# Kernel tuning notes

Hardware: AMD Instinct MI355X
Metric: run time of the kernel (lower is better)

The kernel has to match this reference:

```python
import jax, jax.numpy as jnp
import numpy as np

WS = (7, 7)          # window size
N = WS[0] * WS[1]    # 49 tokens per window
C = 128              # dim
H = 4                # num heads
D = C // H           # head dim = 32
B = 8192             # batch * num_windows
NW = 1024            # windows per image
SCALE = D ** -0.5


def _relative_position_index():
    coords_h = np.arange(WS[0])
    coords_w = np.arange(WS[1])
    coords = np.stack(np.meshgrid(coords_h, coords_w, indexing='ij'))  # [2,Wh,Ww]
    flat = coords.reshape(2, -1)                                        # [2,N]
    rel = flat[:, :, None] - flat[:, None, :]                           # [2,N,N]
    rel = rel.transpose(1, 2, 0).astype(np.int64)                       # [N,N,2]
    rel[:, :, 0] += WS[0] - 1
    rel[:, :, 1] += WS[1] - 1
    rel[:, :, 0] *= 2 * WS[1] - 1
    return rel.sum(-1)                                                  # [N,N]


def setup_inputs() -> dict:
    key = jax.random.key(0)
    ks = jax.random.split(key, 8)
    s = 0.02
    return {
        'x': jax.random.normal(ks[0], (B, N, C), jnp.float32),
        'y': jax.random.normal(ks[1], (B, N, C), jnp.float32),
        'mask': jnp.zeros((NW, N, N), jnp.float32),
        'Wq': jax.random.normal(ks[2], (C, C), jnp.float32) * s,
        'bq': jnp.zeros((C,), jnp.float32),
        'Wkv': jax.random.normal(ks[3], (C, 2 * C), jnp.float32) * s,
        'bkv': jnp.zeros((2 * C,), jnp.float32),
        'bias_table': jax.random.normal(ks[4], ((2 * WS[0] - 1) * (2 * WS[1] - 1), H), jnp.float32) * s,
        'Wp': jax.random.normal(ks[5], (C, C), jnp.float32) * s,
        'bp': jnp.zeros((C,), jnp.float32),
        'rel_idx': jnp.asarray(_relative_position_index(), jnp.int32),
    }


def reference(x, y, mask, Wq, bq, Wkv, bkv, bias_table, Wp, bp, rel_idx):
    b = x.shape[0]
    # q/kv projections
    q = (x @ Wq + bq).reshape(b, N, H, D).transpose(0, 2, 1, 3) * SCALE   # [B,H,N,D]
    kv = (y @ Wkv + bkv).reshape(b, N, 2, H, D).transpose(2, 0, 3, 1, 4)  # [2,B,H,N,D]
    k, v = kv[0], kv[1]
    attn = jnp.einsum('bhnd,bhmd->bhnm', q, k)                            # [B,H,N,N]
    # relative position bias gather
    bias = bias_table[rel_idx.reshape(-1)].reshape(N, N, H).transpose(2, 0, 1)  # [H,N,N]
    attn = attn + bias[None]
    # mask add per window
    nW = mask.shape[0]
    attn = attn.reshape(b // nW, nW, H, N, N) + mask[None, :, None]
    attn = attn.reshape(b, H, N, N)
    attn = jax.nn.softmax(attn, axis=-1)
    out = jnp.einsum('bhnm,bhmd->bhnd', attn, v)                          # [B,H,N,D]
    out = out.transpose(0, 2, 1, 3).reshape(b, N, C)
    return out @ Wp + bp
```

## Files before the change

kernel.cpp:

```cpp
#include <hip/hip_runtime.h>
#include <cstddef>


#define MFMA16 __builtin_amdgcn_mfma_f32_16x16x32_bf16

typedef float f32x4 __attribute__((ext_vector_type(4)));
typedef __bf16 bf16x8 __attribute__((ext_vector_type(8)));
typedef __bf16 bf16x4 __attribute__((ext_vector_type(4)));

constexpr int NTOK = 49;
constexpr int CDIM = 128;
constexpr int NWIN = 1024;
constexpr int NB = 8192;
constexpr float SCALE_F = 0.17677669529663687f;

__device__ __forceinline__ int sw128(int row, int col) {
  return (row << 8) + ((((col >> 3) ^ row) & 15) << 4) + ((col & 7) << 1);
}
__device__ __forceinline__ int sw64(int row, int col) {
  return (row << 7) + ((((col >> 3) ^ (row >> 1)) & 7) << 4) + ((col & 7) << 1);
}
__device__ __forceinline__ int swp(int m, int nl) {
  return (m << 6) + ((((nl >> 3) ^ (m >> 1)) & 3) << 4) + ((nl & 7) << 1);
}

__global__ void prepack_kernel(const float* __restrict__ Wq, const float* __restrict__ Wkv,
                               const float* __restrict__ Wp, const float* __restrict__ bias_table,
                               const int* __restrict__ rel_idx,
                               unsigned short* __restrict__ wFrag, float* __restrict__ biasM) {
  int t = blockIdx.x * 256 + threadIdx.x;
  if (t < 8192) {
    const int mat = t >> 11;
    const int g = t & 2047;
    const int frag = g >> 6, lane = g & 63;
    const int nt = frag >> 2, ks = frag & 3;
    const int li = lane & 15, q4 = lane >> 4;
    const int n = nt * 16 + li;
    bf16x8 tmp;
#pragma unroll
    for (int j = 0; j < 8; ++j) {
      const int k = ks * 32 + q4 * 8 + j;
      float v;
      if (mat == 0) v = Wq[k * 128 + n];
      else if (mat == 1) v = Wkv[k * 256 + n];
      else if (mat == 2) v = Wkv[k * 256 + 128 + n];
      else v = Wp[k * 128 + n];
      tmp[j] = (__bf16)v;
    }
    *(bf16x8*)(wFrag + (size_t)t * 8) = tmp;
  } else {
    const int tb = t - 8192;
    if (tb < 4 * 49 * 64) {
      const int h = tb / 3136;
      const int rem = tb - h * 3136;
      const int m = rem >> 6, n = rem & 63;
      float v = 0.f;
      if (n < NTOK) v = bias_table[rel_idx[m * 49 + n] * 4 + h];
      biasM[tb] = v;
    }
  }
}

__global__ void bmsum_kernel(const float* __restrict__ mask, const float* __restrict__ bias_table,
                             const int* __restrict__ rel_idx, float* __restrict__ bmSum) {
  __shared__ float smk[2401];
  __shared__ int ri[2401];
  __shared__ float bt[169 * 4];
  const int w = blockIdx.x;
  for (int i = threadIdx.x; i < 2401; i += 256) {
    smk[i] = mask[(size_t)w * 2401 + i];
    ri[i] = rel_idx[i];
  }
  for (int i = threadIdx.x; i < 676; i += 256) bt[i] = bias_table[i];
  __syncthreads();
  for (int i = threadIdx.x; i < 3136; i += 256) {
    const int m = i >> 6, n = i & 63;
    const bool valid = (n < NTOK);
    const int mi = m * 49 + (valid ? n : 0);
    const float base = smk[mi];
    const int r = ri[mi];
#pragma unroll
    for (int h = 0; h < 4; ++h) {
      bmSum[((size_t)w * 4 + h) * 3136 + i] = valid ? (bt[r * 4 + h] + base) : -1e30f;
    }
  }
}

template <bool PRESUM>
__global__ __launch_bounds__(256, 3) void attn_kernel(
    const float* __restrict__ x, const float* __restrict__ y, const float* __restrict__ maskp,
    const float* __restrict__ bq, const float* __restrict__ bkv, const float* __restrict__ bp,
    const unsigned short* __restrict__ wFrag, const float* __restrict__ biasM,
    float* __restrict__ out) {
  __shared__ __align__(16) unsigned char lds[32768];
  const int tid = threadIdx.x;
  const int w = tid >> 6;
  const int lane = tid & 63;
  const int li = lane & 15;
  const int q4 = lane >> 4;
  const int b = blockIdx.x;
  const int mh = w >> 1;
  const int nh = w & 1;

  bf16x8 ax[2][4], ay[2][4];
#pragma unroll
  for (int t = 0; t < 2; ++t) {
    const int mrow = mh * 32 + t * 16 + li;
    const int mm = mrow < NTOK ? mrow : 0;
    const float* xr = x + ((size_t)b * NTOK + mm) * CDIM;
    const float* yr = y + ((size_t)b * NTOK + mm) * CDIM;
#pragma unroll
    for (int ks = 0; ks < 4; ++ks) {
      const int c0 = ks * 32 + q4 * 8;
      const float4 a0 = *(const float4*)(xr + c0);
      const float4 a1 = *(const float4*)(xr + c0 + 4);
      const float4 b0 = *(const float4*)(yr + c0);
      const float4 b1 = *(const float4*)(yr + c0 + 4);
      bf16x8 ta, tb;
      ta[0] = (__bf16)a0.x; ta[1] = (__bf16)a0.y; ta[2] = (__bf16)a0.z; ta[3] = (__bf16)a0.w;
      ta[4] = (__bf16)a1.x; ta[5] = (__bf16)a1.y; ta[6] = (__bf16)a1.z; ta[7] = (__bf16)a1.w;
      tb[0] = (__bf16)b0.x; tb[1] = (__bf16)b0.y; tb[2] = (__bf16)b0.z; tb[3] = (__bf16)b0.w;
      tb[4] = (__bf16)b1.x; tb[5] = (__bf16)b1.y; tb[6] = (__bf16)b1.z; tb[7] = (__bf16)b1.w;
      ax[t][ks] = ta;
      ay[t][ks] = tb;
    }
  }

  const unsigned short* wq = wFrag + 0 * 16384 + nh * 8192;
  const unsigned short* wk = wFrag + 1 * 16384 + nh * 8192;
  const unsigned short* wv = wFrag + 2 * 16384 + nh * 8192;
  const unsigned short* wp = wFrag + 3 * 16384 + nh * 8192;
  const unsigned short* mats01[2] = {wq, wk};

  auto ldw = [&](const unsigned short* base, int ntl, bf16x8* dst) {
#pragma unroll
    for (int ks = 0; ks < 4; ++ks)
      dst[ks] = *(const bf16x8*)(base + (ntl * 4 + ks) * 512 + lane * 8);
  };

  bf16x8 wfb[3][4];
  ldw(wq, 0, wfb[0]);
  ldw(wq, 1, wfb[1]);
#pragma unroll
  for (int s = 0; s < 8; ++s) {
    if (s < 6) {
      const int nn = s + 2;
      ldw(mats01[nn >> 2], nn & 3, wfb[nn % 3]);
    }
    const int mat = s >> 2, ntl = s & 3;
    const bf16x8* wf = wfb[s % 3];
    const int ch0 = nh * 64 + ntl * 16 + q4 * 4;
    const float4 b4 = *(const float4*)((mat == 0 ? bq : bkv) + ch0);
    const int ldsoff = (mat == 0) ? 0 : 16384;
#pragma unroll
    for (int t = 0; t < 2; ++t) {
      const bf16x8* af = (mat == 0) ? &ax[t][0] : &ay[t][0];
      f32x4 acc = {0.f, 0.f, 0.f, 0.f};
#pragma unroll
      for (int ks = 0; ks < 4; ++ks) acc = MFMA16(wf[ks], af[ks], acc, 0, 0, 0);
      const int tok = mh * 32 + t * 16 + li;
      bf16x4 pv;
      pv[0] = (__bf16)(acc[0] + b4.x); pv[1] = (__bf16)(acc[1] + b4.y);
      pv[2] = (__bf16)(acc[2] + b4.z); pv[3] = (__bf16)(acc[3] + b4.w);
      *(bf16x4*)(lds + ldsoff + sw128(tok, ch0)) = pv;
    }
  }
  ldw(wv, 0, wfb[0]);
  ldw(wv, 1, wfb[1]);
  __syncthreads();

  const int h = w;
  unsigned char* const pbase = lds + w * 4096;
  bf16x8 aqf[4], bkf[4];
#pragma unroll
  for (int mt = 0; mt < 4; ++mt)
    aqf[mt] = *(const bf16x8*)(lds + sw128(mt * 16 + li, h * 32 + q4 * 8));
#pragma unroll
  for (int nt = 0; nt < 4; ++nt)
    bkf[nt] = *(const bf16x8*)(lds + 16384 + sw128(nt * 16 + li, h * 32 + q4 * 8));

  bf16x4 vpk[2][4];
#pragma unroll
  for (int v = 0; v < 4; ++v) {
    if (v < 2) ldw(wv, v + 2, wfb[(v + 2) % 3]);
    const bf16x8* wf = wfb[v % 3];
    const int nV = nh * 64 + v * 16 + li;
    const float bvv = bkv[128 + nV];
#pragma unroll
    for (int t = 0; t < 2; ++t) {
      f32x4 acc = {0.f, 0.f, 0.f, 0.f};
#pragma unroll
      for (int ks = 0; ks < 4; ++ks) acc = MFMA16(ay[t][ks], wf[ks], acc, 0, 0, 0);
      bf16x4 vv4;
      vv4[0] = (__bf16)(acc[0] + bvv); vv4[1] = (__bf16)(acc[1] + bvv);
      vv4[2] = (__bf16)(acc[2] + bvv); vv4[3] = (__bf16)(acc[3] + bvv);
      vpk[t][v] = vv4;
    }
  }

  const float* __restrict__ bmw =
      PRESUM ? maskp + ((size_t)(b & (NWIN - 1)) * 4 + h) * 3136 : nullptr;
  const float* __restrict__ biasw = biasM + h * 3136;
  const float* __restrict__ maskw =
      PRESUM ? nullptr : maskp + (size_t)(b & (NWIN - 1)) * 2401;

  auto ldbm = [&](int mt, f32x4* dst) {
    const int m = mt * 16 + li;
    const int mm = (m < NTOK ? m : 0);
#pragma unroll
    for (int nt = 0; nt < 4; ++nt) {
      const int nc = nt * 16 + q4 * 4;
      if (PRESUM) {
        dst[nt] = *(const f32x4*)(bmw + mm * 64 + nc);
      } else {
        const f32x4 bv = *(const f32x4*)(biasw + mm * 64 + nc);
        f32x4 mv;
#pragma unroll
        for (int r = 0; r < 4; ++r) {
          const int n = nc + r;
          mv[r] = (n < NTOK) ? maskw[mm * 49 + n] : -1e30f;
        }
        dst[nt] = bv + mv;
      }
    }
  };

  f32x4 bmv[2][4];
  ldbm(0, bmv[0]);
  __syncthreads();

#pragma unroll
  for (int ntl = 0; ntl < 4; ++ntl) {
    const int nV = nh * 64 + ntl * 16 + li;
#pragma unroll
    for (int t = 0; t < 2; ++t)
      *(bf16x4*)(lds + 16384 + sw64(nV, mh * 32 + t * 16 + q4 * 4)) = vpk[t][ntl];
  }

  float inv4[4];
  bf16x4 pHi[4][2];
  const f32x4 zz = {0.f, 0.f, 0.f, 0.f};
#pragma unroll
  for (int mt = 0; mt < 4; ++mt) {
    if (mt < 3) ldbm(mt + 1, bmv[(mt + 1) & 1]);
    f32x4 s4[4];
    __builtin_amdgcn_s_setprio(1);
#pragma unroll
    for (int nt = 0; nt < 4; ++nt) s4[nt] = MFMA16(bkf[nt], aqf[mt], zz, 0, 0, 0);
    __builtin_amdgcn_s_setprio(0);
    const f32x4* bm = bmv[mt & 1];
    float vv[4][4];
    float mx = -3.0e38f;
#pragma unroll
    for (int nt = 0; nt < 4; ++nt)
#pragma unroll
      for (int r = 0; r < 4; ++r) {
        const float tv = fmaf(SCALE_F, s4[nt][r], bm[nt][r]);
        vv[nt][r] = tv;
        mx = fmaxf(mx, tv);
      }
    mx = fmaxf(mx, __shfl_xor(mx, 16));
    mx = fmaxf(mx, __shfl_xor(mx, 32));
    float sm = 0.f;
#pragma unroll
    for (int nt = 0; nt < 4; ++nt)
#pragma unroll
      for (int r = 0; r < 4; ++r) {
        const float e = __expf(vv[nt][r] - mx);
        vv[nt][r] = e;
        sm += e;
      }
    sm += __shfl_xor(sm, 16);
    sm += __shfl_xor(sm, 32);
    inv4[mt] = __builtin_amdgcn_rcpf(sm);
    bf16x4 p0, p1;
    p0[0] = (__bf16)vv[0][0]; p0[1] = (__bf16)vv[0][1];
    p0[2] = (__bf16)vv[0][2]; p0[3] = (__bf16)vv[0][3];
    p1[0] = (__bf16)vv[1][0]; p1[1] = (__bf16)vv[1][1];
    p1[2] = (__bf16)vv[1][2]; p1[3] = (__bf16)vv[1][3];
    *(bf16x4*)(pbase + swp(mt * 16 + li, q4 * 4)) = p0;
    *(bf16x4*)(pbase + swp(mt * 16 + li, 16 + q4 * 4)) = p1;
    bf16x4 h0, h1;
    h0[0] = (__bf16)vv[2][0]; h0[1] = (__bf16)vv[2][1];
    h0[2] = (__bf16)vv[2][2]; h0[3] = (__bf16)vv[2][3];
    h1[0] = (__bf16)vv[3][0]; h1[1] = (__bf16)vv[3][1];
    h1[2] = (__bf16)vv[3][2]; h1[3] = (__bf16)vv[3][3];
    pHi[mt][0] = h0;
    pHi[mt][1] = h1;
  }
  __syncthreads();

  bf16x8 bv2[2][2];
#pragma unroll
  for (int cht = 0; cht < 2; ++cht)
#pragma unroll
    for (int ksn = 0; ksn < 2; ++ksn)
      bv2[cht][ksn] =
          *(const bf16x8*)(lds + 16384 + sw64(h * 32 + cht * 16 + li, ksn * 32 + q4 * 8));
  f32x4 o[2][4];
  {
    bf16x8 ap[4];
#pragma unroll
    for (int mt = 0; mt < 4; ++mt)
      ap[mt] = *(const bf16x8*)(pbase + swp(mt * 16 + li, q4 * 8));
    __builtin_amdgcn_s_setprio(1);
#pragma unroll
    for (int cht = 0; cht < 2; ++cht)
#pragma unroll
      for (int mt = 0; mt < 4; ++mt) o[cht][mt] = MFMA16(bv2[cht][0], ap[mt], zz, 0, 0, 0);
    __builtin_amdgcn_s_setprio(0);
#pragma unroll
    for (int mt = 0; mt < 4; ++mt) {
      *(bf16x4*)(pbase + swp(mt * 16 + li, q4 * 4)) = pHi[mt][0];
      *(bf16x4*)(pbase + swp(mt * 16 + li, 16 + q4 * 4)) = pHi[mt][1];
    }
#pragma unroll
    for (int mt = 0; mt < 4; ++mt)
      ap[mt] = *(const bf16x8*)(pbase + swp(mt * 16 + li, q4 * 8));
    __builtin_amdgcn_s_setprio(1);
#pragma unroll
    for (int cht = 0; cht < 2; ++cht)
#pragma unroll
      for (int mt = 0; mt < 4; ++mt)
        o[cht][mt] = MFMA16(bv2[cht][1], ap[mt], o[cht][mt], 0, 0, 0);
    __builtin_amdgcn_s_setprio(0);
  }
  __syncthreads();

#pragma unroll
  for (int cht = 0; cht < 2; ++cht)
#pragma unroll
    for (int mt = 0; mt < 4; ++mt) {
      bf16x4 zv;
      zv[0] = (__bf16)(o[cht][mt][0] * inv4[mt]);
      zv[1] = (__bf16)(o[cht][mt][1] * inv4[mt]);
      zv[2] = (__bf16)(o[cht][mt][2] * inv4[mt]);
      zv[3] = (__bf16)(o[cht][mt][3] * inv4[mt]);
      *(bf16x4*)(lds + sw128(mt * 16 + li, h * 32 + cht * 16 + q4 * 4)) = zv;
    }
  ldw(wp, 0, wfb[0]);
  ldw(wp, 1, wfb[1]);
  __syncthreads();

  bf16x8 az[2][4];
#pragma unroll
  for (int t = 0; t < 2; ++t)
#pragma unroll
    for (int ks = 0; ks < 4; ++ks)
      az[t][ks] = *(const bf16x8*)(lds + sw128(mh * 32 + t * 16 + li, ks * 32 + q4 * 8));
#pragma unroll
  for (int ntl = 0; ntl < 4; ++ntl) {
    if (ntl < 2) ldw(wp, ntl + 2, wfb[(ntl + 2) % 3]);
    const bf16x8* wf = wfb[ntl % 3];
    const int ch0 = nh * 64 + ntl * 16 + q4 * 4;
    const float4 b4 = *(const float4*)(bp + ch0);
#pragma unroll
    for (int t = 0; t < 2; ++t) {
      f32x4 acc = {0.f, 0.f, 0.f, 0.f};
#pragma unroll
      for (int ks = 0; ks < 4; ++ks) acc = MFMA16(wf[ks], az[t][ks], acc, 0, 0, 0);
      const int tok = mh * 32 + t * 16 + li;
      if (tok < NTOK) {
        float4 st;
        st.x = acc[0] + b4.x; st.y = acc[1] + b4.y;
        st.z = acc[2] + b4.z; st.w = acc[3] + b4.w;
        *(float4*)(out + ((size_t)b * NTOK + tok) * CDIM + ch0) = st;
      }
    }
  }
}

extern "C" void kernel_launch(void* const* d_in, const int* in_sizes, int n_in, void* d_out,
                              int out_size, void* d_ws, size_t ws_size, hipStream_t stream) {
  const float* x = (const float*)d_in[0];
  const float* y = (const float*)d_in[1];
  const float* mask = (const float*)d_in[2];
  const float* Wq = (const float*)d_in[3];
  const float* bq = (const float*)d_in[4];
  const float* Wkv = (const float*)d_in[5];
  const float* bkv = (const float*)d_in[6];
  const float* bt = (const float*)d_in[7];
  const float* Wp = (const float*)d_in[8];
  const float* bp = (const float*)d_in[9];
  const int* rel = (const int*)d_in[10];
  float* out = (float*)d_out;

  unsigned short* wFrag = (unsigned short*)d_ws;
  float* biasM = (float*)((char*)d_ws + 131072);
  float* bmSum = (float*)((char*)d_ws + 181248);
  const size_t needS = 181248 + (size_t)NWIN * 4 * 3136 * sizeof(float);

  prepack_kernel<<<96, 256, 0, stream>>>(Wq, Wkv, Wp, bt, rel, wFrag, biasM);
  if (ws_size >= needS) {
    bmsum_kernel<<<NWIN, 256, 0, stream>>>(mask, bt, rel, bmSum);
    attn_kernel<true><<<NB, 256, 0, stream>>>(x, y, bmSum, bq, bkv, bp, wFrag, biasM, out);
  } else {
    attn_kernel<false><<<NB, 256, 0, stream>>>(x, y, mask, bq, bkv, bp, wFrag, biasM, out);
  }
}
```

Measured before the change: 638.4 us.

## Store presummed bias+mask in fp16 and preload all tiles upfront

The precomputed bias-plus-mask table is now stored as fp16 instead of fp32, which halves the bytes the attention kernel reads per window and head. All four row tiles of that table are loaded into registers before the barrier, replacing the double-buffered per-tile prefetch. Launch bounds are raised from 3 to 4 blocks per CU to push occupancy. The cost is precision loss in the bias and mask values, a -30000 sentinel in place of -1e30 for padded columns, and more register pressure from holding the preloaded values under a tighter register budget.

After: 668.9 us. +4.8%, slower.

```diff
diff --git a/kernel.cpp b/kernel.cpp
--- a/kernel.cpp
+++ b/kernel.cpp
@@ -7,6 +7,7 @@
 typedef float f32x4 __attribute__((ext_vector_type(4)));
 typedef __bf16 bf16x8 __attribute__((ext_vector_type(8)));
 typedef __bf16 bf16x4 __attribute__((ext_vector_type(4)));
+typedef _Float16 f16x4 __attribute__((ext_vector_type(4)));
 
 constexpr int NTOK = 49;
 constexpr int CDIM = 128;
@@ -62,7 +63,7 @@
 }
 
 __global__ void bmsum_kernel(const float* __restrict__ mask, const float* __restrict__ bias_table,
-                             const int* __restrict__ rel_idx, float* __restrict__ bmSum) {
+                             const int* __restrict__ rel_idx, _Float16* __restrict__ bmSum) {
   __shared__ float smk[2401];
   __shared__ int ri[2401];
   __shared__ float bt[169 * 4];
@@ -81,13 +82,14 @@
     const int r = ri[mi];
 #pragma unroll
     for (int h = 0; h < 4; ++h) {
-      bmSum[((size_t)w * 4 + h) * 3136 + i] = valid ? (bt[r * 4 + h] + base) : -1e30f;
+      bmSum[((size_t)w * 4 + h) * 3136 + i] =
+          valid ? (_Float16)(bt[r * 4 + h] + base) : (_Float16)(-30000.0f);
     }
   }
 }
 
 template <bool PRESUM>
-__global__ __launch_bounds__(256, 3) void attn_kernel(
+__global__ __launch_bounds__(256, 4) void attn_kernel(
     const float* __restrict__ x, const float* __restrict__ y, const float* __restrict__ maskp,
     const float* __restrict__ bq, const float* __restrict__ bkv, const float* __restrict__ bp,
     const unsigned short* __restrict__ wFrag, const float* __restrict__ biasM,
@@ -198,21 +200,58 @@
     }
   }
 
-  const float* __restrict__ bmw =
-      PRESUM ? maskp + ((size_t)(b & (NWIN - 1)) * 4 + h) * 3136 : nullptr;
+  const _Float16* __restrict__ bmw =
+      PRESUM ? (const _Float16*)maskp + ((size_t)(b & (NWIN - 1)) * 4 + h) * 3136 : nullptr;
   const float* __restrict__ biasw = biasM + h * 3136;
   const float* __restrict__ maskw =
-      PRESUM ? nullptr : maskp + (size_t)(b & (NWIN - 1)) * 2401;
-
-  auto ldbm = [&](int mt, f32x4* dst) {
-    const int m = mt * 16 + li;
-    const int mm = (m < NTOK ? m : 0);
-#pragma unroll
-    for (int nt = 0; nt < 4; ++nt) {
-      const int nc = nt * 16 + q4 * 4;
-      if (PRESUM) {
-        dst[nt] = *(const f32x4*)(bmw + mm * 64 + nc);
-      } else {
+      PRESUM ? nullptr : (const float*)maskp + (size_t)(b & (NWIN - 1)) * 2401;
+
+  f16x4 bmraw[4][4];
+  if (PRESUM) {
+#pragma unroll
+    for (int mt = 0; mt < 4; ++mt) {
+      const int m = mt * 16 + li;
+      const int mm = (m < NTOK ? m : 0);
+#pragma unroll
+      for (int nt = 0; nt < 4; ++nt)
+        bmraw[mt][nt] = *(const f16x4*)(bmw + mm * 64 + nt * 16 + q4 * 4);
+    }
+  }
+  __syncthreads();
+
+#pragma unroll
+  for (int ntl = 0; ntl < 4; ++ntl) {
+    const int nV = nh * 64 + ntl * 16 + li;
+#pragma unroll
+    for (int t = 0; t < 2; ++t)
+      *(bf16x4*)(lds + 16384 + sw64(nV, mh * 32 + t * 16 + q4 * 4)) = vpk[t][ntl];
+  }
+
+  float inv4[4];
+  bf16x4 pHi[4][2];
+  const f32x4 zz = {0.f, 0.f, 0.f, 0.f};
+#pragma unroll
+  for (int mt = 0; mt < 4; ++mt) {
+    f32x4 s4[4];
+    __builtin_amdgcn_s_setprio(1);
+#pragma unroll
+    for (int nt = 0; nt < 4; ++nt) s4[nt] = MFMA16(bkf[nt], aqf[mt], zz, 0, 0, 0);
+    __builtin_amdgcn_s_setprio(0);
+    f32x4 bm4[4];
+    if (PRESUM) {
+#pragma unroll
+      for (int nt = 0; nt < 4; ++nt) {
+        bm4[nt][0] = (float)bmraw[mt][nt][0];
+        bm4[nt][1] = (float)bmraw[mt][nt][1];
+        bm4[nt][2] = (float)bmraw[mt][nt][2];
+        bm4[nt][3] = (float)bmraw[mt][nt][3];
+      }
+    } else {
+      const int m = mt * 16 + li;
+      const int mm = (m < NTOK ? m : 0);
+#pragma unroll
+      for (int nt = 0; nt < 4; ++nt) {
+        const int nc = nt * 16 + q4 * 4;
         const f32x4 bv = *(const f32x4*)(biasw + mm * 64 + nc);
         f32x4 mv;
 #pragma unroll
@@ -220,42 +259,16 @@
           const int n = nc + r;
           mv[r] = (n < NTOK) ? maskw[mm * 49 + n] : -1e30f;
         }
-        dst[nt] = bv + mv;
+        bm4[nt] = bv + mv;
       }
     }
-  };
-
-  f32x4 bmv[2][4];
-  ldbm(0, bmv[0]);
-  __syncthreads();
-
-#pragma unroll
-  for (int ntl = 0; ntl < 4; ++ntl) {
-    const int nV = nh * 64 + ntl * 16 + li;
-#pragma unroll
-    for (int t = 0; t < 2; ++t)
-      *(bf16x4*)(lds + 16384 + sw64(nV, mh * 32 + t * 16 + q4 * 4)) = vpk[t][ntl];
-  }
-
-  float inv4[4];
-  bf16x4 pHi[4][2];
-  const f32x4 zz = {0.f, 0.f, 0.f, 0.f};
-#pragma unroll
-  for (int mt = 0; mt < 4; ++mt) {
-    if (mt < 3) ldbm(mt + 1, bmv[(mt + 1) & 1]);
-    f32x4 s4[4];
-    __builtin_amdgcn_s_setprio(1);
-#pragma unroll
-    for (int nt = 0; nt < 4; ++nt) s4[nt] = MFMA16(bkf[nt], aqf[mt], zz, 0, 0, 0);
-    __builtin_amdgcn_s_setprio(0);
-    const f32x4* bm = bmv[mt & 1];
     float vv[4][4];
     float mx = -3.0e38f;
 #pragma unroll
     for (int nt = 0; nt < 4; ++nt)
 #pragma unroll
       for (int r = 0; r < 4; ++r) {
-        const float tv = fmaf(SCALE_F, s4[nt][r], bm[nt][r]);
+        const float tv = fmaf(SCALE_F, s4[nt][r], bm4[nt][r]);
         vv[nt][r] = tv;
         mx = fmaxf(mx, tv);
       }
@@ -387,13 +400,14 @@
 
   unsigned short* wFrag = (unsigned short*)d_ws;
   float* biasM = (float*)((char*)d_ws + 131072);
-  float* bmSum = (float*)((char*)d_ws + 181248);
-  const size_t needS = 181248 + (size_t)NWIN * 4 * 3136 * sizeof(float);
+  _Float16* bmSum = (_Float16*)((char*)d_ws + 181248);
+  const size_t needS = 181248 + (size_t)NWIN * 4 * 3136 * sizeof(_Float16);
 
   prepack_kernel<<<96, 256, 0, stream>>>(Wq, Wkv, Wp, bt, rel, wFrag, biasM);
   if (ws_size >= needS) {
     bmsum_kernel<<<NWIN, 256, 0, stream>>>(mask, bt, rel, bmSum);
-    attn_kernel<true><<<NB, 256, 0, stream>>>(x, y, bmSum, bq, bkv, bp, wFrag, biasM, out);
+    attn_kernel<true><<<NB, 256, 0, stream>>>(x, y, (const float*)bmSum, bq, bkv, bp, wFrag,
+                                              biasM, out);
   } else {
     attn_kernel<false><<<NB, 256, 0, stream>>>(x, y, mask, bq, bkv, bp, wFrag, biasM, out);
   }
```
